# Performance work log

Hardware: AMD Instinct MI355X
Metric: run time of the kernel (lower is better)

The kernel has to match this reference:

```python
import jax, jax.numpy as jnp
import numpy as np

NUM_CLASSES = 80
NUM_KERNELS = 256
NUM_GRIDS = (40, 36, 24, 16, 12)
STRIDES = (8, 8, 16, 32, 32)
SCORE_THR = 0.1
MASK_THR = 0.5
UPDATE_THR = 0.05
NMS_PRE = 500
MAX_PER_IMG = 100
NMS_SIGMA = 2.0
ORI_H, ORI_W = 640, 960  # ratio*f_h = 4*160, 4*240 -> upsampled == ori size


def point_nms(heat, kernel=2):
    # torch: hmax = max_pool2d(heat, 2, stride=1, padding=1)[..., :-1, :-1]
    # equivalent: 2x2 window with (1,0) padding top/left, -inf init
    hmax = jax.lax.reduce_window(
        heat, -jnp.inf, jax.lax.max,
        (1, 1, kernel, kernel), (1, 1, 1, 1),
        ((0, 0), (0, 0), (1, 0), (1, 0)))
    return heat * (hmax == heat).astype(heat.dtype)


def setup_inputs() -> dict:
    key = jax.random.key(0)
    ks = jax.random.split(key, 11)
    inp = {}
    for i, g in enumerate(NUM_GRIDS):
        inp[f"cate_p{i}"] = jax.random.normal(ks[i], (1, NUM_CLASSES, g, g), jnp.float32)
        inp[f"kern_p{i}"] = jax.random.normal(ks[5 + i], (1, NUM_KERNELS, g, g), jnp.float32) * 0.05
    inp["mask_feat"] = jax.random.normal(ks[10], (1, NUM_KERNELS, 160, 240), jnp.float32)
    return inp


def _solo_post(cate_list, kern_list, mask_feat):
    # point-NMS on sigmoid scores, flatten grids, concat levels  -> [S, C]
    cate = jnp.concatenate([
        point_nms(jax.nn.sigmoid(c))[0].transpose(1, 2, 0).reshape(-1, NUM_CLASSES)
        for c in cate_list], axis=0)
    kern = jnp.concatenate([
        k[0].transpose(1, 2, 0).reshape(-1, NUM_KERNELS) for k in kern_list], axis=0)
    strides = jnp.concatenate([
        jnp.full((g * g,), float(s), jnp.float32) for g, s in zip(NUM_GRIDS, STRIDES)])

    # score threshold -> fixed-size top-k selection (jit-friendly)
    flat = jnp.where(cate > SCORE_THR, cate, 0.0).reshape(-1)  # [S*C]
    scores, flat_idx = jax.lax.top_k(flat, NMS_PRE)
    grid_idx = flat_idx // NUM_CLASSES
    labels = flat_idx % NUM_CLASSES
    valid = scores > 0.0

    # 1x1 dynamic conv == matmul over channel dim
    kp = kern[grid_idx]                                   # [N, K]
    st = strides[grid_idx]                                # [N]
    seg = jax.nn.sigmoid(jnp.einsum('nk,khw->nhw', kp, mask_feat[0]))  # [N, h, w]
    seg_masks = seg > MASK_THR
    sum_masks = seg_masks.sum((1, 2)).astype(jnp.float32)
    keep = (sum_masks > st) & valid
    seg_score = (seg * seg_masks).sum((1, 2)) / jnp.maximum(sum_masks, 1.0)
    scores = scores * seg_score * keep.astype(scores.dtype)

    # sort descending by updated scores
    order = jnp.argsort(-scores)
    scores = scores[order]
    labels = labels[order]
    seg = seg[order]
    alive = (scores > 0.0).astype(jnp.float32)
    masks_f = seg_masks[order].astype(jnp.float32) * alive[:, None, None]
    sum_m = masks_f.sum((1, 2))

    # matrix NMS (gaussian)
    mflat = masks_f.reshape(NMS_PRE, -1)
    inter = mflat @ mflat.T                               # [N, N]
    union = sum_m[:, None] + sum_m[None, :] - inter
    iou = jnp.triu(jnp.where(union > 0, inter / jnp.maximum(union, 1.0), 0.0), k=1)
    label_m = jnp.triu((labels[:, None] == labels[None, :]).astype(jnp.float32), k=1)
    decay_iou = iou * label_m
    comp_iou = decay_iou.max(axis=0)                      # per instance (column max)
    # decay[i, j] = exp(-sigma*(decay_iou[i,j]^2 - comp_iou[i]^2)); coef = min over i
    decay = jnp.exp(-NMS_SIGMA * (decay_iou ** 2 - comp_iou[:, None] ** 2))
    scores = scores * decay.min(axis=0)

    scores = scores * (scores >= UPDATE_THR).astype(scores.dtype)
    top_s, top_i = jax.lax.top_k(scores, MAX_PER_IMG)
    seg_top = seg[top_i]                                  # [M, h, w]

    # upsample to (f_h*ratio, f_w*ratio) then to ori_size (equal here), crop no-op
    up = jax.image.resize(seg_top, (MAX_PER_IMG, ORI_H, ORI_W), method='bilinear')
    up2 = jax.image.resize(up, (MAX_PER_IMG, ORI_H, ORI_W), method='bilinear')
    return up2, top_s, top_i, labels


def reference(cate_p0, cate_p1, cate_p2, cate_p3, cate_p4,
              kern_p0, kern_p1, kern_p2, kern_p3, kern_p4, mask_feat):
    up2, top_s, top_i, labels = _solo_post(
        [cate_p0, cate_p1, cate_p2, cate_p3, cate_p4],
        [kern_p0, kern_p1, kern_p2, kern_p3, kern_p4], mask_feat)
    pred_masks = up2 > MASK_THR
    return pred_masks, top_s, labels[top_i]
```

## Files before the change

kernel.cpp:

```cpp
#include <hip/hip_runtime.h>
#include <stdint.h>

#define NCLS 80
#define NKER 256
#define STOT 3872
#define NFLAT (STOT*NCLS)
#define NPRE 500
#define NPREP 512
#define MAXI 100
#define MH 160
#define MW 240
#define MP (MH*MW)
#define OH 640
#define OW 960
#define NWORD 600
#define PARTW 300

#define BN 64
#define BP 128
#define BK 32

#define WS_HIST   0u
#define WS_META   262144u
#define WS_ZEROB  266240u
#define WS_IOU    266240u
#define WS_FLAT   2266240u
#define WS_CANDV  3505280u
#define WS_CANDI  3521664u
#define WS_SEL    3538048u
#define WS_KPT    3591296u
#define WS_MB     4115584u
#define WS_PART   6515584u
#define WS_SEG    7715584u

__device__ __forceinline__ float bf2f(unsigned short u) { return __uint_as_float(((unsigned)u) << 16); }
__device__ __forceinline__ unsigned short f2bf(float f) {
  unsigned b = __float_as_uint(f);
  return (unsigned short)((b + 0x7fffu + ((b >> 16) & 1u)) >> 16);
}
__device__ __forceinline__ unsigned fkey(float f) {
  unsigned b = __float_as_uint(f);
  return b ^ ((b & 0x80000000u) ? 0xFFFFFFFFu : 0x80000000u);
}

__global__ __launch_bounds__(256) void k_flat(
    const float* __restrict__ c0, const float* __restrict__ c1, const float* __restrict__ c2,
    const float* __restrict__ c3, const float* __restrict__ c4,
    float* __restrict__ flat, unsigned* __restrict__ hist) {
  int idx = blockIdx.x * 256 + threadIdx.x;
  if (idx >= NFLAT) return;
  int s = idx / NCLS, c = idx - s * NCLS;
  const float* base; int g, cell;
  if (s < 1600)      { base = c0; g = 40; cell = s; }
  else if (s < 2896) { base = c1; g = 36; cell = s - 1600; }
  else if (s < 3472) { base = c2; g = 24; cell = s - 2896; }
  else if (s < 3728) { base = c3; g = 16; cell = s - 3472; }
  else               { base = c4; g = 12; cell = s - 3728; }
  int i = cell / g, j = cell - i * g;
  const float* ch = base + c * g * g;
  float x = ch[i * g + j];
  float m = x;
  if (i > 0 && j > 0) m = fmaxf(m, ch[(i - 1) * g + j - 1]);
  if (i > 0)          m = fmaxf(m, ch[(i - 1) * g + j]);
  if (j > 0)          m = fmaxf(m, ch[i * g + j - 1]);
  bool pass = (x >= m) && ((double)x > -2.1972245773362196 );
  flat[idx] = pass ? x : __int_as_float(0xFF800000);
  if (pass) atomicAdd(&hist[fkey(x) >> 16], 1u);
}

__global__ void k_pivot(const unsigned* __restrict__ hist, unsigned* __restrict__ meta) {
  __shared__ unsigned csum[1024];
  int t = threadIdx.x;
  int hi = 65536 - t * 64, lo = hi - 64;
  unsigned s = 0;
  for (int b = lo; b < hi; ++b) s += hist[b];
  csum[t] = s;
  __syncthreads();
  if (t == 0) {
    unsigned cum = 0;
    for (int cch = 0; cch < 1024; ++cch) {
      if (cum + csum[cch] >= NPRE) {
        int chi = 65536 - cch * 64;
        for (int b = chi - 1; b >= chi - 64; --b) {
          if (cum + hist[b] >= NPRE) { meta[1] = (unsigned)b; return; }
          cum += hist[b];
        }
      }
      cum += csum[cch];
    }
    meta[1] = 0u;
  }
}

__global__ __launch_bounds__(256) void k_compact(
    const float* __restrict__ flat, float* __restrict__ cv, int* __restrict__ ci,
    unsigned* __restrict__ meta) {
  int idx = blockIdx.x * 256 + threadIdx.x;
  if (idx >= NFLAT) return;
  float v = flat[idx];
  if (__float_as_uint(v) == 0xFF800000u) return;
  if ((fkey(v) >> 16) >= meta[1]) {
    unsigned pos = atomicAdd(&meta[0], 1u);
    if (pos < 4096u) { cv[pos] = v; ci[pos] = idx; }
  }
}

__global__ __launch_bounds__(1024) void k_select(
    const float* __restrict__ cv, const int* __restrict__ ci, const unsigned* __restrict__ meta,
    double* __restrict__ sel_score, unsigned* __restrict__ sel_grid,
    unsigned* __restrict__ sel_label, double* __restrict__ sel_stride) {
  __shared__ float sv[4096];
  __shared__ int si[4096];
  int t = threadIdx.x;
  int n = (meta[0] < 4096u) ? (int)meta[0] : 4096;
  for (int i = t; i < 4096; i += 1024) {
    if (i < n) { sv[i] = cv[i]; si[i] = ci[i]; }
    else       { sv[i] = __int_as_float(0xFF800000); si[i] = (1 << 30) + i; }
  }
  __syncthreads();
  for (int k = 2; k <= 4096; k <<= 1)
    for (int j = k >> 1; j > 0; j >>= 1) {
      for (int i = t; i < 4096; i += 1024) {
        int ix = i ^ j;
        if (ix > i) {
          float v1 = sv[i], v2 = sv[ix]; int i1 = si[i], i2 = si[ix];
          bool b2 = (v2 > v1) || (v2 == v1 && i2 < i1);
          bool dir = (i & k) == 0;
          if (dir == b2) { sv[i] = v2; sv[ix] = v1; si[i] = i2; si[ix] = i1; }
        }
      }
      __syncthreads();
    }
  for (int i = t; i < NPREP; i += 1024) {
    if (i < NPRE && i < n) {
      int fidx = si[i];
      unsigned gi = (unsigned)fidx / NCLS;
      sel_score[i] = 1.0 / (1.0 + exp(-(double)sv[i]));
      sel_grid[i] = gi;
      sel_label[i] = (unsigned)fidx - gi * NCLS;
      sel_stride[i] = gi < 2896u ? 8.0 : (gi < 3472u ? 16.0 : 32.0);
    } else {
      sel_score[i] = 0.0; sel_grid[i] = 0u; sel_label[i] = 0u; sel_stride[i] = 1e18;
    }
  }
}

__global__ __launch_bounds__(256) void k_gather(
    const float* __restrict__ k0, const float* __restrict__ k1, const float* __restrict__ k2,
    const float* __restrict__ k3, const float* __restrict__ k4,
    const unsigned* __restrict__ sel_grid, float* __restrict__ kpT) {
  int tid = blockIdx.x * 256 + threadIdx.x;
  if (tid >= NPREP * NKER) return;
  int n = tid & (NPREP - 1);
  int k = tid >> 9;
  float v = 0.f;
  if (n < NPRE) {
    unsigned gi = sel_grid[n];
    const float* base; unsigned g, cell;
    if (gi < 1600u)      { base = k0; g = 40; cell = gi; }
    else if (gi < 2896u) { base = k1; g = 36; cell = gi - 1600u; }
    else if (gi < 3472u) { base = k2; g = 24; cell = gi - 2896u; }
    else if (gi < 3728u) { base = k3; g = 16; cell = gi - 3472u; }
    else                 { base = k4; g = 12; cell = gi - 3728u; }
    v = base[(unsigned)k * g * g + cell];
  }
  kpT[k * NPREP + n] = v;
}

__global__ __launch_bounds__(256, 3) void k_gemm(
    const float* __restrict__ kpT, const float* __restrict__ mf,
    unsigned short* __restrict__ seg, unsigned long long* __restrict__ mb,
    double* __restrict__ part) {
  __shared__ double Asd[BK][BN];
  __shared__ double Bsd[BK][BP];
  int p0 = blockIdx.x * BP, n0 = blockIdx.y * BN;
  int tid = threadIdx.x;
  int tp = tid & 15, tn = tid >> 4;
  double acc[4][8] = {};
  for (int kc = 0; kc < NKER; kc += BK) {
#pragma unroll
    for (int it = 0; it < 4; ++it) {
      int q = it * 256 + tid;
      int row = q >> 5, c2 = q & 31;
      float2 f = *(const float2*)&kpT[(kc + row) * NPREP + n0 + c2 * 2];
      double2 d; d.x = (double)f.x; d.y = (double)f.y;
      *(double2*)&Asd[row][c2 * 2] = d;
    }
#pragma unroll
    for (int it = 0; it < 8; ++it) {
      int q = it * 256 + tid;
      int row = q >> 6, c2 = q & 63;
      float2 f = *(const float2*)&mf[(size_t)(kc + row) * MP + p0 + c2 * 2];
      double2 d; d.x = (double)f.x; d.y = (double)f.y;
      *(double2*)&Bsd[row][c2 * 2] = d;
    }
    __syncthreads();
#pragma unroll 4
    for (int k = 0; k < BK; ++k) {
      double2 a01 = *(double2*)&Asd[k][(tn << 2)];
      double2 a23 = *(double2*)&Asd[k][(tn << 2) + 2];
      double2 b0 = *(double2*)&Bsd[k][tp * 2];
      double2 b1 = *(double2*)&Bsd[k][32 + tp * 2];
      double2 b2 = *(double2*)&Bsd[k][64 + tp * 2];
      double2 b3 = *(double2*)&Bsd[k][96 + tp * 2];
      double a[4] = {a01.x, a01.y, a23.x, a23.y};
      double b[8] = {b0.x, b0.y, b1.x, b1.y, b2.x, b2.y, b3.x, b3.y};
#pragma unroll
      for (int r = 0; r < 4; ++r)
#pragma unroll
        for (int c = 0; c < 8; ++c)
          acc[r][c] = fma(a[r], b[c], acc[r][c]);
    }
    __syncthreads();
  }
  double* partL = (double*)&Asd[0][0];
  unsigned* nibL = (unsigned*)((char*)&Asd[0][0] + 8192);
  for (int r = 0; r < 4; ++r) {
    int nl = (tn << 2) + r;
    int nn = n0 + nl;
    unsigned nb = 0; double wsum = 0.0;
    unsigned short u[8];
#pragma unroll
    for (int c = 0; c < 8; ++c) {
      float z = (float)acc[r][c];
      float sf = 1.0f / (1.0f + __expf(-z));
      u[c] = f2bf(sf);
      if (acc[r][c] > 0.0) { nb |= 1u << c; wsum += (double)sf; }
    }
    if (nn < NPRE) {
#pragma unroll
      for (int g = 0; g < 4; ++g) {
        ushort2 o; o.x = u[2 * g]; o.y = u[2 * g + 1];
        *(ushort2*)&seg[(size_t)nn * MP + p0 + g * 32 + tp * 2] = o;
      }
    }
    partL[nl * 16 + tp] = wsum;
    nibL[nl * 16 + tp] = nb;
  }
  __syncthreads();
  if (tid < 64) {
    int nn = n0 + tid;
    if (nn < NPRE) {
      double ssum = 0.0; unsigned long long w0 = 0ull, w1 = 0ull;
#pragma unroll
      for (int c = 0; c < 16; ++c) {
        ssum += partL[tid * 16 + c];
        unsigned long long nb = (unsigned long long)nibL[tid * 16 + c];
        w0 |= ((nb      & 3ull) << (c * 2)) | (((nb >> 2) & 3ull) << (32 + c * 2));
        w1 |= (((nb >> 4) & 3ull) << (c * 2)) | (((nb >> 6) & 3ull) << (32 + c * 2));
      }
      int bx = blockIdx.x;
      part[nn * PARTW + bx] = ssum;
      mb[nn * NWORD + bx * 2] = w0;
      mb[nn * NWORD + bx * 2 + 1] = w1;
    }
  }
}

__global__ void k_masks(const unsigned long long* __restrict__ mb, const double* __restrict__ part,
                        const double* __restrict__ sel_score, const double* __restrict__ sel_stride,
                        double* __restrict__ summask, double* __restrict__ upd) {
  int n = blockIdx.x, t = threadIdx.x;
  int cnt = 0; double ws = 0.0;
  for (int j = t; j < NWORD; j += 64) cnt += __popcll(mb[n * NWORD + j]);
  for (int j = t; j < PARTW; j += 64) ws += part[n * PARTW + j];
  for (int o = 32; o > 0; o >>= 1) { cnt += __shfl_down(cnt, o); ws += __shfl_down(ws, o); }
  if (t == 0) {
    double cf = (double)cnt;
    double ss = ws / fmax(cf, 1.0);
    double raw = sel_score[n];
    bool keep = (cf > sel_stride[n]) && (raw > 0.0);
    summask[n] = cf;
    upd[n] = keep ? raw * ss : 0.0;
  }
}

__global__ __launch_bounds__(512) void k_sort(
    const double* __restrict__ upd, const unsigned* __restrict__ sel_label, const double* __restrict__ summask,
    double* __restrict__ s_score, unsigned* __restrict__ s_slot, unsigned* __restrict__ s_label2,
    double* __restrict__ s_sum, unsigned* __restrict__ s_alive) {
  __shared__ double sv[NPREP];
  __shared__ int si[NPREP];
  int t = threadIdx.x;
  sv[t] = (t < NPRE) ? upd[t] : -1.0;
  si[t] = t;
  __syncthreads();
  for (int k = 2; k <= NPREP; k <<= 1)
    for (int j = k >> 1; j > 0; j >>= 1) {
      int ix = t ^ j;
      if (ix > t) {
        double v1 = sv[t], v2 = sv[ix]; int i1 = si[t], i2 = si[ix];
        bool b2 = (v2 > v1) || (v2 == v1 && i2 < i1);
        bool dir = (t & k) == 0;
        if (dir == b2) { sv[t] = v2; sv[ix] = v1; si[t] = i2; si[ix] = i1; }
      }
      __syncthreads();
    }
  double sc = sv[t]; int slot = si[t];
  bool alive = sc > 0.0;
  s_score[t] = alive ? sc : 0.0;
  s_slot[t] = (unsigned)slot;
  s_label2[t] = sel_label[slot];
  s_sum[t] = (alive && slot < NPRE) ? summask[slot] : 0.0;
  s_alive[t] = alive ? 1u : 0u;
}

__global__ __launch_bounds__(256) void k_inter(
    const unsigned long long* __restrict__ mb, const unsigned* __restrict__ s_slot,
    const unsigned* __restrict__ s_label2, const unsigned* __restrict__ s_alive,
    const double* __restrict__ s_sum, double* __restrict__ iou) {
  int w = (blockIdx.x * 256 + threadIdx.x) >> 6;
  int lane = threadIdx.x & 63;
  if (w >= NPRE * NPRE) return;
  int i = w / NPRE, j = w - i * NPRE;
  if (i >= j) return;
  double val = 0.0;
  if (s_label2[i] == s_label2[j] && s_alive[i] && s_alive[j]) {
    const unsigned long long* A = mb + (size_t)s_slot[i] * NWORD;
    const unsigned long long* B = mb + (size_t)s_slot[j] * NWORD;
    int c = 0;
    for (int wd = lane; wd < NWORD; wd += 64) c += __popcll(A[wd] & B[wd]);
    for (int o = 32; o > 0; o >>= 1) c += __shfl_down(c, o);
    double inter = (double)c;
    double uni = s_sum[i] + s_sum[j] - inter;
    val = (uni > 0.0) ? inter / fmax(uni, 1.0) : 0.0;
  }
  if (lane == 0) iou[i * NPRE + j] = val;
}

__global__ __launch_bounds__(512) void k_nms_top(
    const double* __restrict__ iou, const double* __restrict__ s_score,
    const unsigned* __restrict__ s_label2, const unsigned* __restrict__ s_slot,
    float* __restrict__ d_out, int maskN, unsigned* __restrict__ up_slot) {
  __shared__ double compS[NPREP];
  __shared__ double sv[NPREP];
  __shared__ int si[NPREP];
  int t = threadIdx.x;
  double cm = 0.0;
  if (t < NPRE)
    for (int i = 0; i < t; ++i) cm = fmax(cm, iou[i * NPRE + t]);
  compS[t] = cm;
  __syncthreads();
  double f = 0.0;
  if (t < NPRE) {
    double m = 0.0;
    for (int i = 0; i < t; ++i) {
      double d = iou[i * NPRE + t];
      m = fmax(m, d * d - compS[i] * compS[i]);
    }
    f = s_score[t] * exp(-2.0 * m);
    if (f < 0.05) f = 0.0;
  }
  sv[t] = f; si[t] = t;
  __syncthreads();
  for (int k = 2; k <= NPREP; k <<= 1)
    for (int j = k >> 1; j > 0; j >>= 1) {
      int ix = t ^ j;
      if (ix > t) {
        double v1 = sv[t], v2 = sv[ix]; int i1 = si[t], i2 = si[ix];
        bool b2 = (v2 > v1) || (v2 == v1 && i2 < i1);
        bool dir = (t & k) == 0;
        if (dir == b2) { sv[t] = v2; sv[ix] = v1; si[t] = i2; si[ix] = i1; }
      }
      __syncthreads();
    }
  if (t < MAXI) {
    int pos = si[t];
    d_out[maskN + t] = (float)sv[t];
    d_out[maskN + MAXI + t] = (float)s_label2[pos];
    up_slot[t] = s_slot[pos];
  }
}

__global__ __launch_bounds__(256) void k_up(const unsigned short* __restrict__ seg,
                                            const unsigned* __restrict__ up_slot,
                                            float* __restrict__ out, int maskN) {
  int o4 = (blockIdx.x * 256 + threadIdx.x) * 4;
  if (o4 >= maskN) return;
  int m = o4 / (OH * OW);
  int rem = o4 - m * (OH * OW);
  int y = rem / OW;
  int x = rem - y * OW;
  int a = x >> 2;
  const unsigned short* row = seg + (size_t)up_slot[m] * MP;
  float sy = y * 0.25f - 0.375f;
  int y0 = (int)floorf(sy);
  float wy = sy - y0;
  int y0c = max(y0, 0), y1c = min(y0 + 1, MH - 1);
  const unsigned short* r0 = row + y0c * MW;
  const unsigned short* r1 = row + y1c * MW;
  int t0 = max(a - 1, 0), t1 = a, t2 = min(a + 1, MW - 1);
  float T0 = bf2f(r0[t0]), T1 = bf2f(r0[t1]), T2 = bf2f(r0[t2]);
  float B0 = bf2f(r1[t0]), B1 = bf2f(r1[t1]), B2 = bf2f(r1[t2]);
  float iwy = 1.f - wy;
  float4 o;
  o.x = iwy * (0.375f * T0 + 0.625f * T1) + wy * (0.375f * B0 + 0.625f * B1);
  o.y = iwy * (0.125f * T0 + 0.875f * T1) + wy * (0.125f * B0 + 0.875f * B1);
  o.z = iwy * (0.875f * T1 + 0.125f * T2) + wy * (0.875f * B1 + 0.125f * B2);
  o.w = iwy * (0.625f * T1 + 0.375f * T2) + wy * (0.625f * B1 + 0.375f * B2);
  o.x = (o.x > 0.5f) ? 1.f : 0.f;
  o.y = (o.y > 0.5f) ? 1.f : 0.f;
  o.z = (o.z > 0.5f) ? 1.f : 0.f;
  o.w = (o.w > 0.5f) ? 1.f : 0.f;
  *(float4*)&out[o4] = o;
}

extern "C" void kernel_launch(void* const* d_in, const int* in_sizes, int n_in,
                              void* d_out, int out_size, void* d_ws, size_t ws_size,
                              hipStream_t stream) {
  const float* c0 = (const float*)d_in[0];
  const float* k0 = (const float*)d_in[1];
  const float* c1 = (const float*)d_in[2];
  const float* k1 = (const float*)d_in[3];
  const float* c2 = (const float*)d_in[4];
  const float* k2 = (const float*)d_in[5];
  const float* c3 = (const float*)d_in[6];
  const float* k3 = (const float*)d_in[7];
  const float* c4 = (const float*)d_in[8];
  const float* k4 = (const float*)d_in[9];
  const float* mf = (const float*)d_in[10];

  char* ws = (char*)d_ws;
  unsigned* hist = (unsigned*)(ws + WS_HIST);
  unsigned* meta = (unsigned*)(ws + WS_META);
  double* iou = (double*)(ws + WS_IOU);
  float* flat = (float*)(ws + WS_FLAT);
  float* cv = (float*)(ws + WS_CANDV);
  int* ci = (int*)(ws + WS_CANDI);
  double* sel_score  = (double*)(ws + WS_SEL + 0);
  unsigned* sel_grid = (unsigned*)(ws + WS_SEL + 4096);
  unsigned* sel_label= (unsigned*)(ws + WS_SEL + 8192);
  double* sel_stride = (double*)(ws + WS_SEL + 12288);
  double* upd        = (double*)(ws + WS_SEL + 16384);
  double* summask    = (double*)(ws + WS_SEL + 20480);
  double* s_score    = (double*)(ws + WS_SEL + 24576);
  unsigned* s_slot   = (unsigned*)(ws + WS_SEL + 28672);
  unsigned* s_label2 = (unsigned*)(ws + WS_SEL + 32768);
  double* s_sum      = (double*)(ws + WS_SEL + 36864);
  unsigned* s_alive  = (unsigned*)(ws + WS_SEL + 40960);
  unsigned* up_slot  = (unsigned*)(ws + WS_SEL + 49152);
  float* kpT = (float*)(ws + WS_KPT);
  unsigned long long* mb = (unsigned long long*)(ws + WS_MB);
  double* part = (double*)(ws + WS_PART);
  unsigned short* seg = (unsigned short*)(ws + WS_SEG);

  int maskN = out_size - 2 * MAXI;

  hipMemsetAsync(ws, 0, WS_ZEROB, stream);

  k_flat<<<(NFLAT + 255) / 256, 256, 0, stream>>>(c0, c1, c2, c3, c4, flat, hist);
  k_pivot<<<1, 1024, 0, stream>>>(hist, meta);
  k_compact<<<(NFLAT + 255) / 256, 256, 0, stream>>>(flat, cv, ci, meta);
  k_select<<<1, 1024, 0, stream>>>(cv, ci, meta, sel_score, sel_grid, sel_label, sel_stride);
  k_gather<<<(NPREP * NKER + 255) / 256, 256, 0, stream>>>(k0, k1, k2, k3, k4, sel_grid, kpT);
  dim3 g6(MP / BP, NPREP / BN);
  k_gemm<<<g6, 256, 0, stream>>>(kpT, mf, seg, mb, part);
  k_masks<<<NPRE, 64, 0, stream>>>(mb, part, sel_score, sel_stride, summask, upd);
  k_sort<<<1, NPREP, 0, stream>>>(upd, sel_label, summask, s_score, s_slot, s_label2, s_sum, s_alive);
  k_inter<<<(NPRE * NPRE) / 4, 256, 0, stream>>>(mb, s_slot, s_label2, s_alive, s_sum, iou);
  k_nms_top<<<1, NPREP, 0, stream>>>(iou, s_score, s_label2, s_slot, (float*)d_out, maskN, up_slot);
  k_up<<<(maskN / 4 + 255) / 256, 256, 0, stream>>>(seg, up_slot, (float*)d_out, maskN);
}
```

Before: 671.2 us.

## Sparse same-label pair list for matrix NMS and register-prefetch GEMM tiles

Replaces the dense 500x500 IoU matrix with a compacted list of alive same-label pairs built in the sort kernel. IoU is computed only for those pairs, and the column maxima and decay maxima are reduced with atomicMax on double bit patterns. The dense 125k-warp launch and the serial per-thread column scans in the single-block NMS kernel go away, at the cost of atomics and one extra launch. The fp64 GEMM also loads the next K-tile into registers while the current tile is computed, hiding global load latency at some register cost.

Result: faster. 600.8 us (-10.5%).

```diff
diff --git a/kernel.cpp b/kernel.cpp
--- a/kernel.cpp
+++ b/kernel.cpp
@@ -22,8 +22,10 @@
 
 #define WS_HIST   0u
 #define WS_META   262144u
-#define WS_ZEROB  266240u
-#define WS_IOU    266240u
+#define WS_CMP    266240u
+#define WS_MDEC   270336u
+#define WS_ZEROB  274432u
+#define WS_PIOU   274432u
 #define WS_FLAT   2266240u
 #define WS_CANDV  3505280u
 #define WS_CANDI  3521664u
@@ -32,6 +34,7 @@
 #define WS_MB     4115584u
 #define WS_PART   6515584u
 #define WS_SEG    7715584u
+#define WS_PLIST  WS_FLAT
 
 __device__ __forceinline__ float bf2f(unsigned short u) { return __uint_as_float(((unsigned)u) << 16); }
 __device__ __forceinline__ unsigned short f2bf(float f) {
@@ -177,24 +180,43 @@
   int tid = threadIdx.x;
   int tp = tid & 15, tn = tid >> 4;
   double acc[4][8] = {};
+  float2 pa[4], pb[8];
+#pragma unroll
+  for (int it = 0; it < 4; ++it) {
+    int q = it * 256 + tid; int row = q >> 5, c2 = q & 31;
+    pa[it] = *(const float2*)&kpT[row * NPREP + n0 + c2 * 2];
+  }
+#pragma unroll
+  for (int it = 0; it < 8; ++it) {
+    int q = it * 256 + tid; int row = q >> 6, c2 = q & 63;
+    pb[it] = *(const float2*)&mf[(size_t)row * MP + p0 + c2 * 2];
+  }
   for (int kc = 0; kc < NKER; kc += BK) {
 #pragma unroll
     for (int it = 0; it < 4; ++it) {
-      int q = it * 256 + tid;
-      int row = q >> 5, c2 = q & 31;
-      float2 f = *(const float2*)&kpT[(kc + row) * NPREP + n0 + c2 * 2];
-      double2 d; d.x = (double)f.x; d.y = (double)f.y;
+      int q = it * 256 + tid; int row = q >> 5, c2 = q & 31;
+      double2 d; d.x = (double)pa[it].x; d.y = (double)pa[it].y;
       *(double2*)&Asd[row][c2 * 2] = d;
     }
 #pragma unroll
     for (int it = 0; it < 8; ++it) {
-      int q = it * 256 + tid;
-      int row = q >> 6, c2 = q & 63;
-      float2 f = *(const float2*)&mf[(size_t)(kc + row) * MP + p0 + c2 * 2];
-      double2 d; d.x = (double)f.x; d.y = (double)f.y;
+      int q = it * 256 + tid; int row = q >> 6, c2 = q & 63;
+      double2 d; d.x = (double)pb[it].x; d.y = (double)pb[it].y;
       *(double2*)&Bsd[row][c2 * 2] = d;
     }
     __syncthreads();
+    if (kc + BK < NKER) {
+#pragma unroll
+      for (int it = 0; it < 4; ++it) {
+        int q = it * 256 + tid; int row = q >> 5, c2 = q & 31;
+        pa[it] = *(const float2*)&kpT[(kc + BK + row) * NPREP + n0 + c2 * 2];
+      }
+#pragma unroll
+      for (int it = 0; it < 8; ++it) {
+        int q = it * 256 + tid; int row = q >> 6, c2 = q & 63;
+        pb[it] = *(const float2*)&mf[(size_t)(kc + BK + row) * MP + p0 + c2 * 2];
+      }
+    }
 #pragma unroll 4
     for (int k = 0; k < BK; ++k) {
       double2 a01 = *(double2*)&Asd[k][(tn << 2)];
@@ -278,9 +300,10 @@
 __global__ __launch_bounds__(512) void k_sort(
     const double* __restrict__ upd, const unsigned* __restrict__ sel_label, const double* __restrict__ summask,
     double* __restrict__ s_score, unsigned* __restrict__ s_slot, unsigned* __restrict__ s_label2,
-    double* __restrict__ s_sum, unsigned* __restrict__ s_alive) {
+    double* __restrict__ s_sum, unsigned* __restrict__ plist, unsigned* __restrict__ meta) {
   __shared__ double sv[NPREP];
   __shared__ int si[NPREP];
+  __shared__ unsigned labv[NPREP];
   int t = threadIdx.x;
   sv[t] = (t < NPRE) ? upd[t] : -1.0;
   si[t] = t;
@@ -298,56 +321,80 @@
     }
   double sc = sv[t]; int slot = si[t];
   bool alive = sc > 0.0;
+  unsigned lab = sel_label[slot];
   s_score[t] = alive ? sc : 0.0;
   s_slot[t] = (unsigned)slot;
-  s_label2[t] = sel_label[slot];
+  s_label2[t] = lab;
   s_sum[t] = (alive && slot < NPRE) ? summask[slot] : 0.0;
-  s_alive[t] = alive ? 1u : 0u;
+  labv[t] = alive ? lab : (0x10000u + (unsigned)t);
+  __syncthreads();
+  if (t < NPRE) {
+    unsigned li = labv[t];
+    if (li < 0x10000u) {
+      for (int j = t + 1; j < NPRE; ++j) {
+        if (labv[j] == li) {
+          unsigned pos = atomicAdd(&meta[2], 1u);
+          plist[pos] = ((unsigned)t << 16) | (unsigned)j;
+        }
+      }
+    }
+  }
 }
 
 __global__ __launch_bounds__(256) void k_inter(
     const unsigned long long* __restrict__ mb, const unsigned* __restrict__ s_slot,
-    const unsigned* __restrict__ s_label2, const unsigned* __restrict__ s_alive,
-    const double* __restrict__ s_sum, double* __restrict__ iou) {
-  int w = (blockIdx.x * 256 + threadIdx.x) >> 6;
+    const double* __restrict__ s_sum, const unsigned* __restrict__ plist,
+    const unsigned* __restrict__ meta, double* __restrict__ piou,
+    unsigned long long* __restrict__ cmp_bits) {
+  int wid = (blockIdx.x * 256 + threadIdx.x) >> 6;
   int lane = threadIdx.x & 63;
-  if (w >= NPRE * NPRE) return;
-  int i = w / NPRE, j = w - i * NPRE;
-  if (i >= j) return;
-  double val = 0.0;
-  if (s_label2[i] == s_label2[j] && s_alive[i] && s_alive[j]) {
+  unsigned npair = meta[2];
+  for (unsigned pp = wid; pp < npair; pp += 256) {
+    unsigned pk = plist[pp];
+    int i = (int)(pk >> 16), j = (int)(pk & 0xFFFFu);
     const unsigned long long* A = mb + (size_t)s_slot[i] * NWORD;
     const unsigned long long* B = mb + (size_t)s_slot[j] * NWORD;
     int c = 0;
     for (int wd = lane; wd < NWORD; wd += 64) c += __popcll(A[wd] & B[wd]);
     for (int o = 32; o > 0; o >>= 1) c += __shfl_down(c, o);
-    double inter = (double)c;
-    double uni = s_sum[i] + s_sum[j] - inter;
-    val = (uni > 0.0) ? inter / fmax(uni, 1.0) : 0.0;
-  }
-  if (lane == 0) iou[i * NPRE + j] = val;
-}
-
-__global__ __launch_bounds__(512) void k_nms_top(
-    const double* __restrict__ iou, const double* __restrict__ s_score,
+    if (lane == 0) {
+      double inter = (double)c;
+      double uni = s_sum[i] + s_sum[j] - inter;
+      double val = (uni > 0.0) ? inter / fmax(uni, 1.0) : 0.0;
+      piou[pp] = val;
+      if (val > 0.0)
+        atomicMax(&cmp_bits[j], (unsigned long long)__double_as_longlong(val));
+    }
+  }
+}
+
+__global__ __launch_bounds__(256) void k_decay(
+    const unsigned* __restrict__ plist, const unsigned* __restrict__ meta,
+    const double* __restrict__ piou, const unsigned long long* __restrict__ cmp_bits,
+    unsigned long long* __restrict__ m_bits) {
+  int idx = blockIdx.x * 256 + threadIdx.x;
+  unsigned npair = meta[2];
+  for (unsigned p = idx; p < npair; p += 2048) {
+    unsigned pk = plist[p];
+    int i = (int)(pk >> 16), j = (int)(pk & 0xFFFFu);
+    double d = piou[p];
+    double ci = __longlong_as_double((long long)cmp_bits[i]);
+    double v = d * d - ci * ci;
+    if (v > 0.0)
+      atomicMax(&m_bits[j], (unsigned long long)__double_as_longlong(v));
+  }
+}
+
+__global__ __launch_bounds__(512) void k_top(
+    const unsigned long long* __restrict__ m_bits, const double* __restrict__ s_score,
     const unsigned* __restrict__ s_label2, const unsigned* __restrict__ s_slot,
     float* __restrict__ d_out, int maskN, unsigned* __restrict__ up_slot) {
-  __shared__ double compS[NPREP];
   __shared__ double sv[NPREP];
   __shared__ int si[NPREP];
   int t = threadIdx.x;
-  double cm = 0.0;
-  if (t < NPRE)
-    for (int i = 0; i < t; ++i) cm = fmax(cm, iou[i * NPRE + t]);
-  compS[t] = cm;
-  __syncthreads();
   double f = 0.0;
   if (t < NPRE) {
-    double m = 0.0;
-    for (int i = 0; i < t; ++i) {
-      double d = iou[i * NPRE + t];
-      m = fmax(m, d * d - compS[i] * compS[i]);
-    }
+    double m = __longlong_as_double((long long)m_bits[t]);
     f = s_score[t] * exp(-2.0 * m);
     if (f < 0.05) f = 0.0;
   }
@@ -423,7 +470,9 @@
   char* ws = (char*)d_ws;
   unsigned* hist = (unsigned*)(ws + WS_HIST);
   unsigned* meta = (unsigned*)(ws + WS_META);
-  double* iou = (double*)(ws + WS_IOU);
+  unsigned long long* cmp_bits = (unsigned long long*)(ws + WS_CMP);
+  unsigned long long* m_bits = (unsigned long long*)(ws + WS_MDEC);
+  double* piou = (double*)(ws + WS_PIOU);
   float* flat = (float*)(ws + WS_FLAT);
   float* cv = (float*)(ws + WS_CANDV);
   int* ci = (int*)(ws + WS_CANDI);
@@ -437,12 +486,12 @@
   unsigned* s_slot   = (unsigned*)(ws + WS_SEL + 28672);
   unsigned* s_label2 = (unsigned*)(ws + WS_SEL + 32768);
   double* s_sum      = (double*)(ws + WS_SEL + 36864);
-  unsigned* s_alive  = (unsigned*)(ws + WS_SEL + 40960);
   unsigned* up_slot  = (unsigned*)(ws + WS_SEL + 49152);
   float* kpT = (float*)(ws + WS_KPT);
   unsigned long long* mb = (unsigned long long*)(ws + WS_MB);
   double* part = (double*)(ws + WS_PART);
   unsigned short* seg = (unsigned short*)(ws + WS_SEG);
+  unsigned* plist = (unsigned*)(ws + WS_PLIST);
 
   int maskN = out_size - 2 * MAXI;
 
@@ -456,8 +505,9 @@
   dim3 g6(MP / BP, NPREP / BN);
   k_gemm<<<g6, 256, 0, stream>>>(kpT, mf, seg, mb, part);
   k_masks<<<NPRE, 64, 0, stream>>>(mb, part, sel_score, sel_stride, summask, upd);
-  k_sort<<<1, NPREP, 0, stream>>>(upd, sel_label, summask, s_score, s_slot, s_label2, s_sum, s_alive);
-  k_inter<<<(NPRE * NPRE) / 4, 256, 0, stream>>>(mb, s_slot, s_label2, s_alive, s_sum, iou);
-  k_nms_top<<<1, NPREP, 0, stream>>>(iou, s_score, s_label2, s_slot, (float*)d_out, maskN, up_slot);
+  k_sort<<<1, NPREP, 0, stream>>>(upd, sel_label, summask, s_score, s_slot, s_label2, s_sum, plist, meta);
+  k_inter<<<64, 256, 0, stream>>>(mb, s_slot, s_sum, plist, meta, piou, cmp_bits);
+  k_decay<<<8, 256, 0, stream>>>(plist, meta, piou, cmp_bits, m_bits);
+  k_top<<<1, NPREP, 0, stream>>>(m_bits, s_score, s_label2, s_slot, (float*)d_out, maskN, up_slot);
   k_up<<<(maskN / 4 + 255) / 256, 256, 0, stream>>>(seg, up_slot, (float*)d_out, maskN);
 }
```
